# Kernel optimization log

Hardware: AMD Instinct MI355X
Metric: run time of the kernel (lower is better)

The kernel has to match this reference:

```python
import jax, jax.numpy as jnp
import numpy as np

B, D, T, K = 32768, 1024, 100, 4  # batch, input_dim, num_trees, 2**(tree_depth-1)

def setup_inputs() -> dict:
    key = jax.random.key(0)
    k1, k2, k3, k4, k5 = jax.random.split(key, 5)
    s1 = 1.0 / np.sqrt(D)
    s2 = 1.0 / np.sqrt(K)
    return {
        "x": jax.random.normal(k1, (B, D), dtype=jnp.float32),
        "W1": jax.random.uniform(k2, (T, K, D), jnp.float32, -s1, s1),  # per-tree first Linear
        "b1": jax.random.uniform(k3, (T, K), jnp.float32, -s1, s1),
        "final_weight": jnp.full((T,), 1.0 / T, dtype=jnp.float32),
        "fc_w": jax.random.uniform(k4, (2, K), jnp.float32, -s2, s2),
        "fc_b": jax.random.uniform(k5, (2,), jnp.float32, -s2, s2),
    }

def reference(x, W1, b1, final_weight, fc_w, fc_b):
    # split_probs for all trees at once: [B, T, K]
    split = jnp.einsum("bd,tkd->btk", x, W1) + b1[None, :, :]
    leaf = jax.nn.sigmoid(split)  # tree[1] is Sigmoid applied to split_probs
    # sum(split.unsqueeze(1)*leaf.unsqueeze(2), -1) == leaf * sum_k(split)
    tree_out = leaf * jnp.sum(split, axis=-1, keepdims=True)  # [B, T, K]
    weighted = jnp.einsum("btk,t->bk", tree_out, final_weight)  # [B, K]
    logits = weighted @ fc_w.T + fc_b  # [B, 2]
    return logits
```

## Files before the change

### kernel.cpp

```cpp
#include <hip/hip_runtime.h>
#include <hip/hip_bf16.h>


typedef __bf16 bf16x8 __attribute__((ext_vector_type(8)));
typedef float f32x4 __attribute__((ext_vector_type(4)));

#define B_ROWS 32768
#define D_DIM  1024
#define N_COLS 400
#define BM     64
#define BK     32
#define NCHUNK 32
#define THREADS 320
#define NTPW 5
#define MT   4

__device__ __forceinline__ unsigned short f2bf(float f) {
    unsigned int u = __float_as_uint(f);
    u += 0x7FFFu + ((u >> 16) & 1u);
    return (unsigned short)(u >> 16);
}
__device__ __forceinline__ unsigned int pk2(float a, float b) {
    return (unsigned int)f2bf(a) | ((unsigned int)f2bf(b) << 16);
}
__device__ __forceinline__ uint4 cvt8u(float4 a, float4 b) {
    uint4 u;
    u.x = pk2(a.x, a.y); u.y = pk2(a.z, a.w);
    u.z = pk2(b.x, b.y); u.w = pk2(b.z, b.w);
    return u;
}
__device__ __forceinline__ bf16x8 cvt8(float4 a, float4 b) {
    return __builtin_bit_cast(bf16x8, cvt8u(a, b));
}

__global__ void cvt_f32_bf16_kernel(const float* __restrict__ in,
                                    unsigned short* __restrict__ out) {
    size_t i = ((size_t)blockIdx.x * 256 + threadIdx.x) * 8;
    float4 v0 = *reinterpret_cast<const float4*>(in + i);
    float4 v1 = *reinterpret_cast<const float4*>(in + i + 4);
    *reinterpret_cast<uint4*>(out + i) = cvt8u(v0, v1);
}

__device__ __forceinline__ void gl_lds16(const unsigned short* g,
                                         unsigned short* l) {
    __builtin_amdgcn_global_load_lds(
        (const __attribute__((address_space(1))) unsigned int*)g,
        (__attribute__((address_space(3))) unsigned int*)l,
        16, 0, 0);
}

#define FOR_N_(OP, m) OP(m,0) OP(m,1) OP(m,2) OP(m,3) OP(m,4)
#define FOR_MN(OP) FOR_N_(OP,0) FOR_N_(OP,1) FOR_N_(OP,2) FOR_N_(OP,3)

#define DECL_ACC(m,n) f32x4 acc##m##n = {};
#define MFMA_MN(m,n) acc##m##n = __builtin_amdgcn_mfma_f32_16x16x32_bf16( \
        afr##m, bfr##n, acc##m##n, 0, 0, 0);

template <int MODE>
__global__ __launch_bounds__(THREADS, 3) void xgb_v9(
    const float* __restrict__ x,
    const void*  __restrict__ b_any,
    const float* __restrict__ b1,
    const float* __restrict__ fw,
    const float* __restrict__ fcw,
    const float* __restrict__ fcb,
    float* __restrict__ out)
{
    __shared__ __align__(16) unsigned short Abuf[2][BM * BK];
    __shared__ __align__(16) unsigned short Bbuf[2][N_COLS * BK];
    __shared__ float Pbuf[BM * NTPW * 2];

    const int tid  = threadIdx.x;
    const int wave = tid >> 6;
    const int lane = tid & 63;
    const int quad = lane >> 4;
    const int l15  = lane & 15;
    const int nf   = wave;
    const int row0 = blockIdx.x * BM;

    FOR_MN(DECL_ACC)

    if (MODE == 0) {
        const unsigned short* w1b = (const unsigned short*)b_any;

#define BDECL(t) const unsigned short* bsrc##t; int bdst##t; \
        { const int s_ = wave + 5 * (t); const int rb_ = s_ * 16 + (lane >> 2); \
          const int cc_ = ((lane & 3) - (rb_ >> 1)) & 3; \
          bsrc##t = w1b + (size_t)rb_ * D_DIM + cc_ * 8; \
          bdst##t = s_ * 512; }
        BDECL(0) BDECL(1) BDECL(2) BDECL(3) BDECL(4)

        const int r0a = tid >> 2, c0a = tid & 3;
        const bool doA = (tid < 256);
        const float* asrc0 = x + (size_t)(row0 + r0a) * D_DIM + c0a * 8;
        const int adst0 = r0a * 32 + ((c0a + (r0a >> 1)) & 3) * 8;
        float4 areg00, areg01;

#define LOADA(kc) do { if (doA) { \
        areg00 = *reinterpret_cast<const float4*>(asrc0 + (kc));     \
        areg01 = *reinterpret_cast<const float4*>(asrc0 + (kc) + 4); \
        } } while (0)

#define WRITEA(Ab) do { if (doA) \
        *reinterpret_cast<uint4*>((Ab) + adst0) = cvt8u(areg00, areg01); \
        } while (0)

#define STAGEB(kc, Bb) do { \
        gl_lds16(bsrc0 + (kc), (Bb) + bdst0); \
        gl_lds16(bsrc1 + (kc), (Bb) + bdst1); \
        gl_lds16(bsrc2 + (kc), (Bb) + bdst2); \
        gl_lds16(bsrc3 + (kc), (Bb) + bdst3); \
        gl_lds16(bsrc4 + (kc), (Bb) + bdst4); } while (0)

#define LOAD_AFR(m) { const int row_ = (m) * 16 + l15; \
        const int p_ = (quad + (row_ >> 1)) & 3; \
        afr##m = *reinterpret_cast<const bf16x8*>(Ab_ + row_ * 32 + p_ * 8); }
#define LOAD_BFR(n) { const int row_ = (nf * NTPW + (n)) * 16 + l15; \
        const int p_ = (quad + (row_ >> 1)) & 3; \
        bfr##n = *reinterpret_cast<const bf16x8*>(Bb_ + row_ * 32 + p_ * 8); }

        LOADA(0);
        STAGEB(0, Bbuf[0]);
        WRITEA(Abuf[0]);

        #pragma unroll 1
        for (int c = 0; c < NCHUNK; ++c) {
            const int cur = c & 1;
            const unsigned short* Ab_ = Abuf[cur];
            const unsigned short* Bb_ = Bbuf[cur];
            __syncthreads();
            if (c + 1 < NCHUNK) {
                LOADA((c + 1) * BK);
                STAGEB((c + 1) * BK, Bbuf[1 - cur]);
            }
            {
                bf16x8 afr0, afr1, afr2, afr3;
                bf16x8 bfr0, bfr1, bfr2, bfr3, bfr4;
                LOAD_AFR(0) LOAD_AFR(1) LOAD_AFR(2) LOAD_AFR(3)
                LOAD_BFR(0) LOAD_BFR(1) LOAD_BFR(2) LOAD_BFR(3) LOAD_BFR(4)
                FOR_MN(MFMA_MN)
            }
            if (c + 1 < NCHUNK) WRITEA(Abuf[1 - cur]);
        }
    } else {
        const float* af = x + (size_t)(row0 + l15) * D_DIM + quad * 8;
        const float* bf32 = (const float*)b_any
                          + (size_t)((nf * NTPW) * 16 + l15) * D_DIM + quad * 8;
        for (int step = 0; step < 32; ++step) {
            const int off = step * 32;
            bf16x8 afr0, afr1, afr2, afr3;
            bf16x8 bfr0, bfr1, bfr2, bfr3, bfr4;
#define LOAD_AFR2(m) { \
            float4 a0_ = *reinterpret_cast<const float4*>(af + (size_t)(m) * 16 * D_DIM + off); \
            float4 a1_ = *reinterpret_cast<const float4*>(af + (size_t)(m) * 16 * D_DIM + off + 4); \
            afr##m = cvt8(a0_, a1_); }
#define LOAD_BFR2(n) { \
            float4 b0_ = *reinterpret_cast<const float4*>(bf32 + (size_t)(n) * 16 * D_DIM + off); \
            float4 b1_ = *reinterpret_cast<const float4*>(bf32 + (size_t)(n) * 16 * D_DIM + off + 4); \
            bfr##n = cvt8(b0_, b1_); }
            LOAD_AFR2(0) LOAD_AFR2(1) LOAD_AFR2(2) LOAD_AFR2(3)
            LOAD_BFR2(0) LOAD_BFR2(1) LOAD_BFR2(2) LOAD_BFR2(3) LOAD_BFR2(4)
            FOR_MN(MFMA_MN)
        }
    }

    const float fcw0 = fcw[l15 & 3];
    const float fcw1 = fcw[4 + (l15 & 3)];

#define PRE_N(n) \
    const float bias##n = b1[(nf * NTPW + (n)) * 16 + l15]; \
    const float tw##n   = fw[((nf * NTPW + (n)) * 16 + l15) >> 2];
    PRE_N(0) PRE_N(1) PRE_N(2) PRE_N(3) PRE_N(4)

#define EPI_TERM(m,r,n) { \
        const float split_ = acc##m##n[r] + bias##n; \
        float s_ = split_; \
        s_ += __shfl_xor(s_, 1); \
        s_ += __shfl_xor(s_, 2); \
        const float leaf_ = 1.0f / (1.0f + __expf(-split_)); \
        const float val_ = tw##n * leaf_ * s_; \
        q0 += val_ * fcw0; q1 += val_ * fcw1; }

#define EPI_ONE(m,r) { \
        float q0 = 0.f, q1 = 0.f; \
        EPI_TERM(m,r,0) EPI_TERM(m,r,1) EPI_TERM(m,r,2) \
        EPI_TERM(m,r,3) EPI_TERM(m,r,4) \
        q0 += __shfl_xor(q0, 1); q0 += __shfl_xor(q0, 2); \
        q0 += __shfl_xor(q0, 4); q0 += __shfl_xor(q0, 8); \
        q1 += __shfl_xor(q1, 1); q1 += __shfl_xor(q1, 2); \
        q1 += __shfl_xor(q1, 4); q1 += __shfl_xor(q1, 8); \
        const int row_ = (m) * 16 + quad * 4 + (r);            \
        if (l15 == 0) Pbuf[(row_ * NTPW + nf) * 2 + 0] = q0; \
        if (l15 == 1) Pbuf[(row_ * NTPW + nf) * 2 + 1] = q1; }

#define EPI_M(m) EPI_ONE(m,0) EPI_ONE(m,1) EPI_ONE(m,2) EPI_ONE(m,3)
    EPI_M(0) EPI_M(1) EPI_M(2) EPI_M(3)

    __syncthreads();

    if (tid < 2 * BM) {
        const int r = tid >> 1, j = tid & 1;
        float s = fcb[j];
        #pragma unroll
        for (int w = 0; w < NTPW; ++w)
            s += Pbuf[(r * NTPW + w) * 2 + j];
        out[(row0 + r) * 2 + j] = s;
    }
}

extern "C" void kernel_launch(void* const* d_in, const int* in_sizes, int n_in,
                              void* d_out, int out_size, void* d_ws, size_t ws_size,
                              hipStream_t stream) {
    const float* x   = (const float*)d_in[0];
    const float* W1  = (const float*)d_in[1];
    const float* b1  = (const float*)d_in[2];
    const float* fw  = (const float*)d_in[3];
    const float* fcw = (const float*)d_in[4];
    const float* fcb = (const float*)d_in[5];
    float* out = (float*)d_out;

    const size_t w1_elems = (size_t)N_COLS * D_DIM;
    if (ws_size >= w1_elems * sizeof(unsigned short)) {
        unsigned short* w1b = (unsigned short*)d_ws;
        cvt_f32_bf16_kernel<<<(int)(w1_elems / 2048), 256, 0, stream>>>(W1, w1b);
        xgb_v9<0><<<B_ROWS / BM, THREADS, 0, stream>>>(
            x, (const void*)w1b, b1, fw, fcw, fcb, out);
    } else {
        xgb_v9<2><<<B_ROWS / BM, THREADS, 0, stream>>>(
            x, (const void*)W1, b1, fw, fcw, fcb, out);
    }
}
```

Baseline: 265.6 us.

## Drop LDS staging; load MFMA fragments directly from global with register double-buffering

Removes the shared-memory double buffers for A and B and has each wave load its MFMA fragments straight from global memory into registers, with a software-pipelined X/Y register ping-pong across the fully unrolled K loop. The block doubles to 640 threads, split into two M-halves of 32 rows times five N groups, so each wave computes 2x5 tiles instead of 4x5. This removes __syncthreads barriers and LDS traffic from the main loop. In exchange, each x row is fetched by five waves and each W1 slice by two waves, so L2/global traffic per block rises, and register pressure grows from the double-buffered fragments.

```diff
diff --git a/kernel.cpp b/kernel.cpp
--- a/kernel.cpp
+++ b/kernel.cpp
@@ -9,11 +9,10 @@
 #define D_DIM  1024
 #define N_COLS 400
 #define BM     64
-#define BK     32
 #define NCHUNK 32
-#define THREADS 320
+#define THREADS 640
 #define NTPW 5
-#define MT   4
+#define MT   2
 
 __device__ __forceinline__ unsigned short f2bf(float f) {
     unsigned int u = __float_as_uint(f);
@@ -41,23 +40,15 @@
     *reinterpret_cast<uint4*>(out + i) = cvt8u(v0, v1);
 }
 
-__device__ __forceinline__ void gl_lds16(const unsigned short* g,
-                                         unsigned short* l) {
-    __builtin_amdgcn_global_load_lds(
-        (const __attribute__((address_space(1))) unsigned int*)g,
-        (__attribute__((address_space(3))) unsigned int*)l,
-        16, 0, 0);
-}
-
 #define FOR_N_(OP, m) OP(m,0) OP(m,1) OP(m,2) OP(m,3) OP(m,4)
-#define FOR_MN(OP) FOR_N_(OP,0) FOR_N_(OP,1) FOR_N_(OP,2) FOR_N_(OP,3)
+#define FOR_MN(OP) FOR_N_(OP,0) FOR_N_(OP,1)
 
 #define DECL_ACC(m,n) f32x4 acc##m##n = {};
 #define MFMA_MN(m,n) acc##m##n = __builtin_amdgcn_mfma_f32_16x16x32_bf16( \
         afr##m, bfr##n, acc##m##n, 0, 0, 0);
 
 template <int MODE>
-__global__ __launch_bounds__(THREADS, 3) void xgb_v9(
+__global__ __launch_bounds__(THREADS, 1) void xgb_v12(
     const float* __restrict__ x,
     const void*  __restrict__ b_any,
     const float* __restrict__ b1,
@@ -66,8 +57,6 @@
     const float* __restrict__ fcb,
     float* __restrict__ out)
 {
-    __shared__ __align__(16) unsigned short Abuf[2][BM * BK];
-    __shared__ __align__(16) unsigned short Bbuf[2][N_COLS * BK];
     __shared__ float Pbuf[BM * NTPW * 2];
 
     const int tid  = threadIdx.x;
@@ -75,7 +64,8 @@
     const int lane = tid & 63;
     const int quad = lane >> 4;
     const int l15  = lane & 15;
-    const int nf   = wave;
+    const int mh   = wave / 5;
+    const int nf   = wave % 5;
     const int row0 = blockIdx.x * BM;
 
     FOR_MN(DECL_ACC)
@@ -83,83 +73,71 @@
     if (MODE == 0) {
         const unsigned short* w1b = (const unsigned short*)b_any;
 
-#define BDECL(t) const unsigned short* bsrc##t; int bdst##t; \
-        { const int s_ = wave + 5 * (t); const int rb_ = s_ * 16 + (lane >> 2); \
-          const int cc_ = ((lane & 3) - (rb_ >> 1)) & 3; \
-          bsrc##t = w1b + (size_t)rb_ * D_DIM + cc_ * 8; \
-          bdst##t = s_ * 512; }
-        BDECL(0) BDECL(1) BDECL(2) BDECL(3) BDECL(4)
-
-        const int r0a = tid >> 2, c0a = tid & 3;
-        const bool doA = (tid < 256);
-        const float* asrc0 = x + (size_t)(row0 + r0a) * D_DIM + c0a * 8;
-        const int adst0 = r0a * 32 + ((c0a + (r0a >> 1)) & 3) * 8;
-        float4 areg00, areg01;
-
-#define LOADA(kc) do { if (doA) { \
-        areg00 = *reinterpret_cast<const float4*>(asrc0 + (kc));     \
-        areg01 = *reinterpret_cast<const float4*>(asrc0 + (kc) + 4); \
-        } } while (0)
-
-#define WRITEA(Ab) do { if (doA) \
-        *reinterpret_cast<uint4*>((Ab) + adst0) = cvt8u(areg00, areg01); \
+        const float* pa0 = x + (size_t)(row0 + mh * 32 + l15) * D_DIM + quad * 8;
+        const float* pa1 = pa0 + (size_t)16 * D_DIM;
+        const unsigned short* pb0 = w1b + (size_t)((nf * NTPW + 0) * 16 + l15) * D_DIM + quad * 8;
+        const unsigned short* pb1 = pb0 + (size_t)16 * D_DIM;
+        const unsigned short* pb2 = pb1 + (size_t)16 * D_DIM;
+        const unsigned short* pb3 = pb2 + (size_t)16 * D_DIM;
+        const unsigned short* pb4 = pb3 + (size_t)16 * D_DIM;
+
+        float4 arX00, arX01, arX10, arX11;
+        float4 arY00, arY01, arY10, arY11;
+        uint4  brX0, brX1, brX2, brX3, brX4;
+        uint4  brY0, brY1, brY2, brY3, brY4;
+
+#define GLOADS(S, c) do { \
+        ar##S##00 = *reinterpret_cast<const float4*>(pa0 + (c) * 32);     \
+        ar##S##01 = *reinterpret_cast<const float4*>(pa0 + (c) * 32 + 4); \
+        ar##S##10 = *reinterpret_cast<const float4*>(pa1 + (c) * 32);     \
+        ar##S##11 = *reinterpret_cast<const float4*>(pa1 + (c) * 32 + 4); \
+        br##S##0  = *reinterpret_cast<const uint4*>(pb0 + (c) * 32);      \
+        br##S##1  = *reinterpret_cast<const uint4*>(pb1 + (c) * 32);      \
+        br##S##2  = *reinterpret_cast<const uint4*>(pb2 + (c) * 32);      \
+        br##S##3  = *reinterpret_cast<const uint4*>(pb3 + (c) * 32);      \
+        br##S##4  = *reinterpret_cast<const uint4*>(pb4 + (c) * 32);      \
         } while (0)
 
-#define STAGEB(kc, Bb) do { \
-        gl_lds16(bsrc0 + (kc), (Bb) + bdst0); \
-        gl_lds16(bsrc1 + (kc), (Bb) + bdst1); \
-        gl_lds16(bsrc2 + (kc), (Bb) + bdst2); \
-        gl_lds16(bsrc3 + (kc), (Bb) + bdst3); \
-        gl_lds16(bsrc4 + (kc), (Bb) + bdst4); } while (0)
-
-#define LOAD_AFR(m) { const int row_ = (m) * 16 + l15; \
-        const int p_ = (quad + (row_ >> 1)) & 3; \
-        afr##m = *reinterpret_cast<const bf16x8*>(Ab_ + row_ * 32 + p_ * 8); }
-#define LOAD_BFR(n) { const int row_ = (nf * NTPW + (n)) * 16 + l15; \
-        const int p_ = (quad + (row_ >> 1)) & 3; \
-        bfr##n = *reinterpret_cast<const bf16x8*>(Bb_ + row_ * 32 + p_ * 8); }
-
-        LOADA(0);
-        STAGEB(0, Bbuf[0]);
-        WRITEA(Abuf[0]);
-
-        #pragma unroll 1
+#define COMPUTE(S) do { \
+        bf16x8 afr0 = cvt8(ar##S##00, ar##S##01); \
+        bf16x8 afr1 = cvt8(ar##S##10, ar##S##11); \
+        bf16x8 bfr0 = __builtin_bit_cast(bf16x8, br##S##0); \
+        bf16x8 bfr1 = __builtin_bit_cast(bf16x8, br##S##1); \
+        bf16x8 bfr2 = __builtin_bit_cast(bf16x8, br##S##2); \
+        bf16x8 bfr3 = __builtin_bit_cast(bf16x8, br##S##3); \
+        bf16x8 bfr4 = __builtin_bit_cast(bf16x8, br##S##4); \
+        FOR_MN(MFMA_MN) \
+        } while (0)
+
+#define PAIR(c) GLOADS(Y, (c) + 1); COMPUTE(X); \
+                GLOADS(X, (c) + 2); COMPUTE(Y);
+
+        GLOADS(X, 0);
+        PAIR(0)  PAIR(2)  PAIR(4)  PAIR(6)  PAIR(8)
+        PAIR(10) PAIR(12) PAIR(14) PAIR(16) PAIR(18)
+        PAIR(20) PAIR(22) PAIR(24) PAIR(26) PAIR(28)
+        GLOADS(Y, 31); COMPUTE(X); COMPUTE(Y);
+    } else {
+        const float* paf0 = x + (size_t)(row0 + mh * 32 + l15) * D_DIM + quad * 8;
+        const float* paf1 = paf0 + (size_t)16 * D_DIM;
+        const float* pbf0 = (const float*)b_any
+                          + (size_t)((nf * NTPW + 0) * 16 + l15) * D_DIM + quad * 8;
+        const float* pbf1 = pbf0 + (size_t)16 * D_DIM;
+        const float* pbf2 = pbf1 + (size_t)16 * D_DIM;
+        const float* pbf3 = pbf2 + (size_t)16 * D_DIM;
+        const float* pbf4 = pbf3 + (size_t)16 * D_DIM;
+        #pragma unroll 2
         for (int c = 0; c < NCHUNK; ++c) {
-            const int cur = c & 1;
-            const unsigned short* Ab_ = Abuf[cur];
-            const unsigned short* Bb_ = Bbuf[cur];
-            __syncthreads();
-            if (c + 1 < NCHUNK) {
-                LOADA((c + 1) * BK);
-                STAGEB((c + 1) * BK, Bbuf[1 - cur]);
-            }
-            {
-                bf16x8 afr0, afr1, afr2, afr3;
-                bf16x8 bfr0, bfr1, bfr2, bfr3, bfr4;
-                LOAD_AFR(0) LOAD_AFR(1) LOAD_AFR(2) LOAD_AFR(3)
-                LOAD_BFR(0) LOAD_BFR(1) LOAD_BFR(2) LOAD_BFR(3) LOAD_BFR(4)
-                FOR_MN(MFMA_MN)
-            }
-            if (c + 1 < NCHUNK) WRITEA(Abuf[1 - cur]);
-        }
-    } else {
-        const float* af = x + (size_t)(row0 + l15) * D_DIM + quad * 8;
-        const float* bf32 = (const float*)b_any
-                          + (size_t)((nf * NTPW) * 16 + l15) * D_DIM + quad * 8;
-        for (int step = 0; step < 32; ++step) {
-            const int off = step * 32;
-            bf16x8 afr0, afr1, afr2, afr3;
+            const int off = c * 32;
+            bf16x8 afr0, afr1;
             bf16x8 bfr0, bfr1, bfr2, bfr3, bfr4;
-#define LOAD_AFR2(m) { \
-            float4 a0_ = *reinterpret_cast<const float4*>(af + (size_t)(m) * 16 * D_DIM + off); \
-            float4 a1_ = *reinterpret_cast<const float4*>(af + (size_t)(m) * 16 * D_DIM + off + 4); \
-            afr##m = cvt8(a0_, a1_); }
-#define LOAD_BFR2(n) { \
-            float4 b0_ = *reinterpret_cast<const float4*>(bf32 + (size_t)(n) * 16 * D_DIM + off); \
-            float4 b1_ = *reinterpret_cast<const float4*>(bf32 + (size_t)(n) * 16 * D_DIM + off + 4); \
-            bfr##n = cvt8(b0_, b1_); }
-            LOAD_AFR2(0) LOAD_AFR2(1) LOAD_AFR2(2) LOAD_AFR2(3)
-            LOAD_BFR2(0) LOAD_BFR2(1) LOAD_BFR2(2) LOAD_BFR2(3) LOAD_BFR2(4)
+            afr0 = cvt8(*reinterpret_cast<const float4*>(paf0 + off),
+                        *reinterpret_cast<const float4*>(paf0 + off + 4));
+            afr1 = cvt8(*reinterpret_cast<const float4*>(paf1 + off),
+                        *reinterpret_cast<const float4*>(paf1 + off + 4));
+#define LBF2(n) bfr##n = cvt8(*reinterpret_cast<const float4*>(pbf##n + off), \
+                              *reinterpret_cast<const float4*>(pbf##n + off + 4));
+            LBF2(0) LBF2(1) LBF2(2) LBF2(3) LBF2(4)
             FOR_MN(MFMA_MN)
         }
     }
@@ -189,12 +167,12 @@
         q0 += __shfl_xor(q0, 4); q0 += __shfl_xor(q0, 8); \
         q1 += __shfl_xor(q1, 1); q1 += __shfl_xor(q1, 2); \
         q1 += __shfl_xor(q1, 4); q1 += __shfl_xor(q1, 8); \
-        const int row_ = (m) * 16 + quad * 4 + (r);            \
+        const int row_ = mh * 32 + (m) * 16 + quad * 4 + (r);    \
         if (l15 == 0) Pbuf[(row_ * NTPW + nf) * 2 + 0] = q0; \
         if (l15 == 1) Pbuf[(row_ * NTPW + nf) * 2 + 1] = q1; }
 
 #define EPI_M(m) EPI_ONE(m,0) EPI_ONE(m,1) EPI_ONE(m,2) EPI_ONE(m,3)
-    EPI_M(0) EPI_M(1) EPI_M(2) EPI_M(3)
+    EPI_M(0) EPI_M(1)
 
     __syncthreads();
 
@@ -223,10 +201,10 @@
     if (ws_size >= w1_elems * sizeof(unsigned short)) {
         unsigned short* w1b = (unsigned short*)d_ws;
         cvt_f32_bf16_kernel<<<(int)(w1_elems / 2048), 256, 0, stream>>>(W1, w1b);
-        xgb_v9<0><<<B_ROWS / BM, THREADS, 0, stream>>>(
+        xgb_v12<0><<<B_ROWS / BM, THREADS, 0, stream>>>(
             x, (const void*)w1b, b1, fw, fcw, fcb, out);
     } else {
-        xgb_v9<2><<<B_ROWS / BM, THREADS, 0, stream>>>(
+        xgb_v12<2><<<B_ROWS / BM, THREADS, 0, stream>>>(
             x, (const void*)W1, b1, fw, fcw, fcb, out);
     }
 }
```

New measurement: 334.8 us. 1.26x slower.

## Pad weight columns to 512, use 8 waves, prefetch A two chunks ahead

Applied to the files above, without the earlier changes.

The converted bf16 weight matrix is zero-padded from 400 to 512 columns so each of 8 waves owns 4 N-tiles, giving 512 threads per block instead of 320. The x tile is now prefetched into two alternating register sets two chunks ahead. The blanket __syncthreads is replaced by explicit vmcnt/lgkmcnt waits, a raw s_barrier and sched_barriers, so the next chunk's loads stay in flight across the barrier. The cost is wasted MFMA work on the padded columns, duplicate x loads by the upper 256 threads, and lower occupancy (launch bounds of 2 blocks per CU instead of 3).

```diff
diff --git a/kernel.cpp b/kernel.cpp
--- a/kernel.cpp
+++ b/kernel.cpp
@@ -8,11 +8,12 @@
 #define B_ROWS 32768
 #define D_DIM  1024
 #define N_COLS 400
+#define NPAD   512
 #define BM     64
 #define BK     32
 #define NCHUNK 32
-#define THREADS 320
-#define NTPW 5
+#define THREADS 512
+#define NTPW 4
 #define MT   4
 
 __device__ __forceinline__ unsigned short f2bf(float f) {
@@ -33,12 +34,17 @@
     return __builtin_bit_cast(bf16x8, cvt8u(a, b));
 }
 
-__global__ void cvt_f32_bf16_kernel(const float* __restrict__ in,
+__global__ void cvt_pad_bf16_kernel(const float* __restrict__ in,
                                     unsigned short* __restrict__ out) {
     size_t i = ((size_t)blockIdx.x * 256 + threadIdx.x) * 8;
-    float4 v0 = *reinterpret_cast<const float4*>(in + i);
-    float4 v1 = *reinterpret_cast<const float4*>(in + i + 4);
-    *reinterpret_cast<uint4*>(out + i) = cvt8u(v0, v1);
+    if (i < (size_t)N_COLS * D_DIM) {
+        float4 v0 = *reinterpret_cast<const float4*>(in + i);
+        float4 v1 = *reinterpret_cast<const float4*>(in + i + 4);
+        *reinterpret_cast<uint4*>(out + i) = cvt8u(v0, v1);
+    } else {
+        uint4 z; z.x = z.y = z.z = z.w = 0u;
+        *reinterpret_cast<uint4*>(out + i) = z;
+    }
 }
 
 __device__ __forceinline__ void gl_lds16(const unsigned short* g,
@@ -49,7 +55,7 @@
         16, 0, 0);
 }
 
-#define FOR_N_(OP, m) OP(m,0) OP(m,1) OP(m,2) OP(m,3) OP(m,4)
+#define FOR_N_(OP, m) OP(m,0) OP(m,1) OP(m,2) OP(m,3)
 #define FOR_MN(OP) FOR_N_(OP,0) FOR_N_(OP,1) FOR_N_(OP,2) FOR_N_(OP,3)
 
 #define DECL_ACC(m,n) f32x4 acc##m##n = {};
@@ -57,7 +63,7 @@
         afr##m, bfr##n, acc##m##n, 0, 0, 0);
 
 template <int MODE>
-__global__ __launch_bounds__(THREADS, 3) void xgb_v9(
+__global__ __launch_bounds__(THREADS, 2) void xgb_v13(
     const float* __restrict__ x,
     const void*  __restrict__ b_any,
     const float* __restrict__ b1,
@@ -67,8 +73,8 @@
     float* __restrict__ out)
 {
     __shared__ __align__(16) unsigned short Abuf[2][BM * BK];
-    __shared__ __align__(16) unsigned short Bbuf[2][N_COLS * BK];
-    __shared__ float Pbuf[BM * NTPW * 2];
+    __shared__ __align__(16) unsigned short Bbuf[2][NPAD * BK];
+    __shared__ float Pbuf[BM * 8 * 2];
 
     const int tid  = threadIdx.x;
     const int wave = tid >> 6;
@@ -84,33 +90,34 @@
         const unsigned short* w1b = (const unsigned short*)b_any;
 
 #define BDECL(t) const unsigned short* bsrc##t; int bdst##t; \
-        { const int s_ = wave + 5 * (t); const int rb_ = s_ * 16 + (lane >> 2); \
+        { const int s_ = wave + 8 * (t); const int rb_ = s_ * 16 + (lane >> 2); \
           const int cc_ = ((lane & 3) - (rb_ >> 1)) & 3; \
           bsrc##t = w1b + (size_t)rb_ * D_DIM + cc_ * 8; \
           bdst##t = s_ * 512; }
-        BDECL(0) BDECL(1) BDECL(2) BDECL(3) BDECL(4)
-
-        const int r0a = tid >> 2, c0a = tid & 3;
-        const bool doA = (tid < 256);
-        const float* asrc0 = x + (size_t)(row0 + r0a) * D_DIM + c0a * 8;
-        const int adst0 = r0a * 32 + ((c0a + (r0a >> 1)) & 3) * 8;
-        float4 areg00, areg01;
-
-#define LOADA(kc) do { if (doA) { \
-        areg00 = *reinterpret_cast<const float4*>(asrc0 + (kc));     \
-        areg01 = *reinterpret_cast<const float4*>(asrc0 + (kc) + 4); \
-        } } while (0)
-
-#define WRITEA(Ab) do { if (doA) \
-        *reinterpret_cast<uint4*>((Ab) + adst0) = cvt8u(areg00, areg01); \
-        } while (0)
+        BDECL(0) BDECL(1) BDECL(2) BDECL(3)
 
 #define STAGEB(kc, Bb) do { \
         gl_lds16(bsrc0 + (kc), (Bb) + bdst0); \
         gl_lds16(bsrc1 + (kc), (Bb) + bdst1); \
         gl_lds16(bsrc2 + (kc), (Bb) + bdst2); \
-        gl_lds16(bsrc3 + (kc), (Bb) + bdst3); \
-        gl_lds16(bsrc4 + (kc), (Bb) + bdst4); } while (0)
+        gl_lds16(bsrc3 + (kc), (Bb) + bdst3); } while (0)
+
+        const int slot = tid & 255;
+        const int r0a = slot >> 2, c0a = slot & 3;
+        const float* asrc0 = x + (size_t)(row0 + r0a) * D_DIM + c0a * 8;
+        const int adst0 = r0a * 32 + ((c0a + (r0a >> 1)) & 3) * 8;
+        float4 a0lo, a0hi, a1lo, a1hi;
+
+#define LOADA0(kc) do { \
+        a0lo = *reinterpret_cast<const float4*>(asrc0 + (kc));     \
+        a0hi = *reinterpret_cast<const float4*>(asrc0 + (kc) + 4); } while (0)
+#define LOADA1(kc) do { \
+        a1lo = *reinterpret_cast<const float4*>(asrc0 + (kc));     \
+        a1hi = *reinterpret_cast<const float4*>(asrc0 + (kc) + 4); } while (0)
+#define WRITEA0(Ab) do { \
+        *reinterpret_cast<uint4*>((Ab) + adst0) = cvt8u(a0lo, a0hi); } while (0)
+#define WRITEA1(Ab) do { \
+        *reinterpret_cast<uint4*>((Ab) + adst0) = cvt8u(a1lo, a1hi); } while (0)
 
 #define LOAD_AFR(m) { const int row_ = (m) * 16 + l15; \
         const int p_ = (quad + (row_ >> 1)) & 3; \
@@ -119,47 +126,65 @@
         const int p_ = (quad + (row_ >> 1)) & 3; \
         bfr##n = *reinterpret_cast<const bf16x8*>(Bb_ + row_ * 32 + p_ * 8); }
 
-        LOADA(0);
         STAGEB(0, Bbuf[0]);
-        WRITEA(Abuf[0]);
+        __builtin_amdgcn_sched_barrier(0);
+        LOADA0(0);
+        WRITEA0(Abuf[0]);
+        __builtin_amdgcn_sched_barrier(0);
+        LOADA1(BK);
 
         #pragma unroll 1
         for (int c = 0; c < NCHUNK; ++c) {
             const int cur = c & 1;
             const unsigned short* Ab_ = Abuf[cur];
             const unsigned short* Bb_ = Bbuf[cur];
-            __syncthreads();
+            if (c == NCHUNK - 1) {
+                asm volatile("s_waitcnt vmcnt(0)" ::: "memory");
+            } else {
+                asm volatile("s_waitcnt vmcnt(2)" ::: "memory");
+            }
+            asm volatile("s_waitcnt lgkmcnt(0)" ::: "memory");
+            __builtin_amdgcn_s_barrier();
+            __builtin_amdgcn_sched_barrier(0);
             if (c + 1 < NCHUNK) {
-                LOADA((c + 1) * BK);
                 STAGEB((c + 1) * BK, Bbuf[1 - cur]);
+                __builtin_amdgcn_sched_barrier(0);
+                if (c + 2 < NCHUNK) {
+                    if (cur == 0) LOADA0((c + 2) * BK);
+                    else          LOADA1((c + 2) * BK);
+                }
+                __builtin_amdgcn_sched_barrier(0);
             }
             {
                 bf16x8 afr0, afr1, afr2, afr3;
-                bf16x8 bfr0, bfr1, bfr2, bfr3, bfr4;
+                bf16x8 bfr0, bfr1, bfr2, bfr3;
                 LOAD_AFR(0) LOAD_AFR(1) LOAD_AFR(2) LOAD_AFR(3)
-                LOAD_BFR(0) LOAD_BFR(1) LOAD_BFR(2) LOAD_BFR(3) LOAD_BFR(4)
+                LOAD_BFR(0) LOAD_BFR(1) LOAD_BFR(2) LOAD_BFR(3)
                 FOR_MN(MFMA_MN)
             }
-            if (c + 1 < NCHUNK) WRITEA(Abuf[1 - cur]);
+            if (c + 1 < NCHUNK) {
+                if (cur == 0) WRITEA1(Abuf[1]);
+                else          WRITEA0(Abuf[0]);
+            }
         }
     } else {
         const float* af = x + (size_t)(row0 + l15) * D_DIM + quad * 8;
-        const float* bf32 = (const float*)b_any
-                          + (size_t)((nf * NTPW) * 16 + l15) * D_DIM + quad * 8;
-        for (int step = 0; step < 32; ++step) {
-            const int off = step * 32;
+#define PBF(n) const float* pbf##n; { \
+        int r_ = (nf * NTPW + (n)) * 16 + l15; if (r_ > N_COLS - 1) r_ = 0; \
+        pbf##n = (const float*)b_any + (size_t)r_ * D_DIM + quad * 8; }
+        PBF(0) PBF(1) PBF(2) PBF(3)
+        for (int step = 0; step < NCHUNK; ++step) {
+            const int off = step * BK;
             bf16x8 afr0, afr1, afr2, afr3;
-            bf16x8 bfr0, bfr1, bfr2, bfr3, bfr4;
-#define LOAD_AFR2(m) { \
-            float4 a0_ = *reinterpret_cast<const float4*>(af + (size_t)(m) * 16 * D_DIM + off); \
-            float4 a1_ = *reinterpret_cast<const float4*>(af + (size_t)(m) * 16 * D_DIM + off + 4); \
-            afr##m = cvt8(a0_, a1_); }
-#define LOAD_BFR2(n) { \
-            float4 b0_ = *reinterpret_cast<const float4*>(bf32 + (size_t)(n) * 16 * D_DIM + off); \
-            float4 b1_ = *reinterpret_cast<const float4*>(bf32 + (size_t)(n) * 16 * D_DIM + off + 4); \
-            bfr##n = cvt8(b0_, b1_); }
-            LOAD_AFR2(0) LOAD_AFR2(1) LOAD_AFR2(2) LOAD_AFR2(3)
-            LOAD_BFR2(0) LOAD_BFR2(1) LOAD_BFR2(2) LOAD_BFR2(3) LOAD_BFR2(4)
+            bf16x8 bfr0, bfr1, bfr2, bfr3;
+#define LAF2(m) afr##m = cvt8( \
+            *reinterpret_cast<const float4*>(af + (size_t)(m) * 16 * D_DIM + off), \
+            *reinterpret_cast<const float4*>(af + (size_t)(m) * 16 * D_DIM + off + 4));
+#define LBF2(n) bfr##n = cvt8( \
+            *reinterpret_cast<const float4*>(pbf##n + off), \
+            *reinterpret_cast<const float4*>(pbf##n + off + 4));
+            LAF2(0) LAF2(1) LAF2(2) LAF2(3)
+            LBF2(0) LBF2(1) LBF2(2) LBF2(3)
             FOR_MN(MFMA_MN)
         }
     }
@@ -168,9 +193,11 @@
     const float fcw1 = fcw[4 + (l15 & 3)];
 
 #define PRE_N(n) \
-    const float bias##n = b1[(nf * NTPW + (n)) * 16 + l15]; \
-    const float tw##n   = fw[((nf * NTPW + (n)) * 16 + l15) >> 2];
-    PRE_N(0) PRE_N(1) PRE_N(2) PRE_N(3) PRE_N(4)
+    const int  col##n  = (nf * NTPW + (n)) * 16 + l15; \
+    const bool ok##n   = (col##n < N_COLS); \
+    const float bias##n = ok##n ? b1[ok##n ? col##n : 0] : 0.0f; \
+    const float tw##n   = ok##n ? fw[ok##n ? (col##n >> 2) : 0] : 0.0f;
+    PRE_N(0) PRE_N(1) PRE_N(2) PRE_N(3)
 
 #define EPI_TERM(m,r,n) { \
         const float split_ = acc##m##n[r] + bias##n; \
@@ -183,15 +210,14 @@
 
 #define EPI_ONE(m,r) { \
         float q0 = 0.f, q1 = 0.f; \
-        EPI_TERM(m,r,0) EPI_TERM(m,r,1) EPI_TERM(m,r,2) \
-        EPI_TERM(m,r,3) EPI_TERM(m,r,4) \
+        EPI_TERM(m,r,0) EPI_TERM(m,r,1) EPI_TERM(m,r,2) EPI_TERM(m,r,3) \
         q0 += __shfl_xor(q0, 1); q0 += __shfl_xor(q0, 2); \
         q0 += __shfl_xor(q0, 4); q0 += __shfl_xor(q0, 8); \
         q1 += __shfl_xor(q1, 1); q1 += __shfl_xor(q1, 2); \
         q1 += __shfl_xor(q1, 4); q1 += __shfl_xor(q1, 8); \
         const int row_ = (m) * 16 + quad * 4 + (r);            \
-        if (l15 == 0) Pbuf[(row_ * NTPW + nf) * 2 + 0] = q0; \
-        if (l15 == 1) Pbuf[(row_ * NTPW + nf) * 2 + 1] = q1; }
+        if (l15 == 0) Pbuf[(row_ * 8 + nf) * 2 + 0] = q0; \
+        if (l15 == 1) Pbuf[(row_ * 8 + nf) * 2 + 1] = q1; }
 
 #define EPI_M(m) EPI_ONE(m,0) EPI_ONE(m,1) EPI_ONE(m,2) EPI_ONE(m,3)
     EPI_M(0) EPI_M(1) EPI_M(2) EPI_M(3)
@@ -202,8 +228,8 @@
         const int r = tid >> 1, j = tid & 1;
         float s = fcb[j];
         #pragma unroll
-        for (int w = 0; w < NTPW; ++w)
-            s += Pbuf[(r * NTPW + w) * 2 + j];
+        for (int w = 0; w < 8; ++w)
+            s += Pbuf[(r * 8 + w) * 2 + j];
         out[(row0 + r) * 2 + j] = s;
     }
 }
@@ -219,14 +245,14 @@
     const float* fcb = (const float*)d_in[5];
     float* out = (float*)d_out;
 
-    const size_t w1_elems = (size_t)N_COLS * D_DIM;
-    if (ws_size >= w1_elems * sizeof(unsigned short)) {
+    const size_t pad_elems = (size_t)NPAD * D_DIM;
+    if (ws_size >= pad_elems * sizeof(unsigned short)) {
         unsigned short* w1b = (unsigned short*)d_ws;
-        cvt_f32_bf16_kernel<<<(int)(w1_elems / 2048), 256, 0, stream>>>(W1, w1b);
-        xgb_v9<0><<<B_ROWS / BM, THREADS, 0, stream>>>(
+        cvt_pad_bf16_kernel<<<(int)(pad_elems / 2048), 256, 0, stream>>>(W1, w1b);
+        xgb_v13<0><<<B_ROWS / BM, THREADS, 0, stream>>>(
             x, (const void*)w1b, b1, fw, fcw, fcb, out);
     } else {
-        xgb_v9<2><<<B_ROWS / BM, THREADS, 0, stream>>>(
+        xgb_v13<2><<<B_ROWS / BM, THREADS, 0, stream>>>(
             x, (const void*)W1, b1, fw, fcw, fcb, out);
     }
 }
```

Measured after the change: 276.2 us. 4.0% more time.
